# Kernel optimization log

Hardware: AMD Instinct MI355X
Metric: run time of the kernel (lower is better)

Reference implementation:

```python
import jax, jax.numpy as jnp
import numpy as np

B, CIN, COUT, T, K = 8, 64, 64, 16384, 127


def setup_inputs() -> dict:
    key = jax.random.key(0)
    kx, kw = jax.random.split(key)
    x = jax.random.normal(kx, (B, CIN, T), dtype=jnp.float32)
    sigma = np.sqrt(2.0 / (CIN * K + COUT)).astype(np.float32)
    W = jax.random.normal(kw, (COUT, CIN, K), dtype=jnp.float32) * sigma
    return {"x": x, "W": W}


def reference(x, W):
    # Full linear convolution via FFT (true convolution, matches
    # torchaudio.functional.fftconvolve), summed over in_channels,
    # then trimmed to mode='same' (output length == T, centered).
    T_ = x.shape[-1]
    K_ = W.shape[-1]
    n = T_ + K_ - 1  # linear-conv length, no circular wraparound
    Xf = jnp.fft.rfft(x, n=n)   # [B, Cin, nf] complex
    Wf = jnp.fft.rfft(W, n=n)   # [Cout, Cin, nf] complex
    # Batched complex multiply-accumulate over in_channels (single pass,
    # no per-output-channel redundant FFTs).
    Yf = jnp.einsum('bif,oif->bof', Xf, Wf)  # [B, Cout, nf]
    y_full = jnp.fft.irfft(Yf, n=n)          # [B, Cout, T+K-1]
    start = (K_ - 1) // 2                    # 'same': centered crop
    return y_full[..., start:start + T_]
```

## Files before the change

### kernel.cpp

```cpp
#include <hip/hip_runtime.h>

#define T_LEN 16384
#define CIN   64
#define COUT  64
#define KTAPS 127
#define TN    512
#define XROWS 640
#define WT_KS 4096

typedef __attribute__((ext_vector_type(8)))  __bf16 bf16x8;
typedef __attribute__((ext_vector_type(16))) float  f32x16;
typedef __attribute__((ext_vector_type(4)))  float  float4v;

__device__ inline unsigned short f2bf(float f) {
    unsigned u = __builtin_bit_cast(unsigned, f);
    u += 0x7fffu + ((u >> 16) & 1u);
    return (unsigned short)(u >> 16);
}

__global__ void wt_transform(const float* __restrict__ W,
                             unsigned short* __restrict__ Wt) {
    int tid = blockIdx.x * 256 + threadIdx.x;
    int o = tid >> 6, i = tid & 63;
    int cc = i >> 4, kg = (i >> 3) & 1, e = i & 7, m = o >> 5, l31 = o & 31;
    int hw = ((cc * 2 + m) * 64 + kg * 32 + l31) * 8 + e;
    const float* src = W + tid * KTAPS;
    unsigned short* dst = Wt + hw;
    for (int kp = 0; kp < KTAPS; ++kp)
        dst[kp * WT_KS] = f2bf(src[126 - kp]);
}

#define GLL16(g, l)                                                        \
    __builtin_amdgcn_global_load_lds(                                      \
        (const __attribute__((address_space(1))) void*)(g),                \
        (__attribute__((address_space(3))) void*)(l), 16, 0, 0)

__global__ __launch_bounds__(512, 2)
void conv_mfma(const float* __restrict__ x,
               const unsigned short* __restrict__ Wt,
               float* __restrict__ y) {
    __shared__ __align__(16) char pool[114688];
    unsigned short* xs = (unsigned short*)pool;
    char* asbase = pool + 81920;

    const int tid = threadIdx.x;
    const int bb  = blockIdx.x >> 5;
    const int tt  = blockIdx.x & 31;
    const int t0  = tt * TN;

    {
        const int cin = tid >> 3;
        const int s   = tid & 7;
        const float* xrow = x + (bb * CIN + cin) * T_LEN;
        const int p = cin >> 2, c3 = cin & 3;
        for (int j = 0; j < 20; ++j) {
            const int w = 32 * j + 4 * s;
            const int u = t0 - 64 + w;
            float4v v;
            if (u >= 0 && u + 4 <= T_LEN) {
                v = *(const float4v*)(xrow + u);
            } else {
                v.x = (u + 0 >= 0 && u + 0 < T_LEN) ? xrow[u + 0] : 0.f;
                v.y = (u + 1 >= 0 && u + 1 < T_LEN) ? xrow[u + 1] : 0.f;
                v.z = (u + 2 >= 0 && u + 2 < T_LEN) ? xrow[u + 2] : 0.f;
                v.w = (u + 3 >= 0 && u + 3 < T_LEN) ? xrow[u + 3] : 0.f;
            }
            #pragma unroll
            for (int e = 0; e < 4; ++e) {
                const int we = w + e;
                const float fv = (e == 0) ? v.x : (e == 1) ? v.y : (e == 2) ? v.z : v.w;
                xs[we * 64 + ((p ^ (we & 15)) << 2) + c3] = f2bf(fv);
            }
        }
    }

    auto stageA = [&](int k0, int k1, int buf) {
        #pragma unroll
        for (int h = 0; h < 2; ++h) {
            const int c   = tid + h * 512;
            const int q   = c >> 9;
            const int off = (c & 511) * 16;
            const char* g = (const char*)(Wt + (q ? k1 : k0) * WT_KS) + off;
            char* l = asbase + buf * 16384 + q * 8192 + off;
            GLL16(g, l);
        }
    };

    stageA(0, 64, 0);
    asm volatile("s_waitcnt vmcnt(0)" ::: "memory");
    __syncthreads();

    const int lane   = tid & 63;
    const int wv     = tid >> 6;
    const int quad   = wv >> 2;
    const int ww     = wv & 3;
    const int l31    = lane & 31;
    const int kg     = lane >> 5;
    const int twbase = ww * 128;
    const int brow0  = twbase + l31 + 1;

    f32x16 acc[2][4] = {};

    auto phase = [&](int p, int buf) {
        if (p + 1 < 64) {
            int k1 = 64 + p + 1; if (k1 > 126) k1 = 126;
            stageA(p + 1, k1, buf ^ 1);
        }
        const int kp = quad ? 64 + p : p;
        if (quad == 0 || p < 63) {
            const char* aslice = asbase + buf * 16384 + quad * 8192;
            const int rb   = brow0 + kp;
            const int rb15 = rb & 15;
            const char* xrowp = (const char*)xs + rb * 128;
            #pragma unroll
            for (int cc = 0; cc < 4; ++cc) {
                bf16x8 a0 = *(const bf16x8*)(aslice + ((cc * 2 + 0) * 64 + lane) * 16);
                bf16x8 a1 = *(const bf16x8*)(aslice + ((cc * 2 + 1) * 64 + lane) * 16);
                const int o0 = (((4 * cc + 2 * kg + 0) ^ rb15) << 3);
                const int o1 = (((4 * cc + 2 * kg + 1) ^ rb15) << 3);
                #pragma unroll
                for (int n = 0; n < 4; ++n) {
                    uint2 lo = *(const uint2*)(xrowp + n * 4096 + o0);
                    uint2 hi = *(const uint2*)(xrowp + n * 4096 + o1);
                    uint4 t4 = {lo.x, lo.y, hi.x, hi.y};
                    bf16x8 b = __builtin_bit_cast(bf16x8, t4);
                    acc[0][n] = __builtin_amdgcn_mfma_f32_32x32x16_bf16(a0, b, acc[0][n], 0, 0, 0);
                    acc[1][n] = __builtin_amdgcn_mfma_f32_32x32x16_bf16(a1, b, acc[1][n], 0, 0, 0);
                }
            }
        }
        asm volatile("s_waitcnt vmcnt(0)" ::: "memory");
        __builtin_amdgcn_s_barrier();
    };

    for (int p = 0; p < 64; p += 2) {
        phase(p + 0, 0);
        phase(p + 1, 1);
    }

    __syncthreads();
    float* msm = (float*)pool;
    #pragma unroll
    for (int m = 0; m < 2; ++m) {
        if (quad == 1) {
            #pragma unroll
            for (int n = 0; n < 4; ++n)
                #pragma unroll
                for (int r = 0; r < 16; ++r)
                    msm[(n * 16 + r) * 256 + ww * 64 + lane] = acc[m][n][r];
        }
        __syncthreads();
        if (quad == 0) {
            #pragma unroll
            for (int n = 0; n < 4; ++n)
                #pragma unroll
                for (int r = 0; r < 16; ++r)
                    acc[m][n][r] += msm[(n * 16 + r) * 256 + ww * 64 + lane];
        }
        __syncthreads();
    }

    if (quad == 0) {
        const int ybase = (bb * COUT) * T_LEN;
        #pragma unroll
        for (int m = 0; m < 2; ++m) {
            #pragma unroll
            for (int n = 0; n < 4; ++n) {
                const int t = t0 + twbase + n * 32 + l31;
                #pragma unroll
                for (int r = 0; r < 16; ++r) {
                    const int o = m * 32 + (r & 3) + 8 * (r >> 2) + 4 * kg;
                    y[ybase + o * T_LEN + t] = acc[m][n][r];
                }
            }
        }
    }
}

extern "C" void kernel_launch(void* const* d_in, const int* in_sizes, int n_in,
                              void* d_out, int out_size, void* d_ws, size_t ws_size,
                              hipStream_t stream) {
    const float* x = (const float*)d_in[0];
    const float* W = (const float*)d_in[1];
    float* yout = (float*)d_out;
    unsigned short* Wt = (unsigned short*)d_ws;

    wt_transform<<<16, 256, 0, stream>>>(W, Wt);

    const int grid = 8 * (T_LEN / TN);
    conv_mfma<<<grid, 512, 0, stream>>>(x, Wt, yout);
}
```

Before: 130.9 us.

## Load weight fragments directly to registers instead of staging through LDS

Replaces the LDS double-buffered weight staging (global_load_lds plus per-tap barriers) with direct global-to-register loads of the A fragments, double-buffered in registers across taps. This removes the per-tap workgroup barrier and the LDS A-buffer, shrinking shared memory. Each wave now issues its own global loads (duplicated across the four waves per quad), and more VGPRs are used, which may pressure occupancy under the 512x2 launch bound.

Result: faster. 125.9 us (-3.8%).

```diff
diff --git a/kernel.cpp b/kernel.cpp
--- a/kernel.cpp
+++ b/kernel.cpp
@@ -30,18 +30,12 @@
         dst[kp * WT_KS] = f2bf(src[126 - kp]);
 }
 
-#define GLL16(g, l)                                                        \
-    __builtin_amdgcn_global_load_lds(                                      \
-        (const __attribute__((address_space(1))) void*)(g),                \
-        (__attribute__((address_space(3))) void*)(l), 16, 0, 0)
-
 __global__ __launch_bounds__(512, 2)
 void conv_mfma(const float* __restrict__ x,
                const unsigned short* __restrict__ Wt,
                float* __restrict__ y) {
-    __shared__ __align__(16) char pool[114688];
+    __shared__ __align__(16) char pool[81920];
     unsigned short* xs = (unsigned short*)pool;
-    char* asbase = pool + 81920;
 
     const int tid = threadIdx.x;
     const int bb  = blockIdx.x >> 5;
@@ -74,22 +68,6 @@
         }
     }
 
-    auto stageA = [&](int k0, int k1, int buf) {
-        #pragma unroll
-        for (int h = 0; h < 2; ++h) {
-            const int c   = tid + h * 512;
-            const int q   = c >> 9;
-            const int off = (c & 511) * 16;
-            const char* g = (const char*)(Wt + (q ? k1 : k0) * WT_KS) + off;
-            char* l = asbase + buf * 16384 + q * 8192 + off;
-            GLL16(g, l);
-        }
-    };
-
-    stageA(0, 64, 0);
-    asm volatile("s_waitcnt vmcnt(0)" ::: "memory");
-    __syncthreads();
-
     const int lane   = tid & 63;
     const int wv     = tid >> 6;
     const int quad   = wv >> 2;
@@ -99,43 +77,48 @@
     const int twbase = ww * 128;
     const int brow0  = twbase + l31 + 1;
 
+    const int kp0  = quad ? 64 : 0;
+    const int ntap = quad ? 63 : 64;
+
+    const char* ab = (const char*)Wt + lane * 16;
+
     f32x16 acc[2][4] = {};
+    uint4 a0r[8], a1r[8];
 
-    auto phase = [&](int p, int buf) {
-        if (p + 1 < 64) {
-            int k1 = 64 + p + 1; if (k1 > 126) k1 = 126;
-            stageA(p + 1, k1, buf ^ 1);
-        }
-        const int kp = quad ? 64 + p : p;
-        if (quad == 0 || p < 63) {
-            const char* aslice = asbase + buf * 16384 + quad * 8192;
-            const int rb   = brow0 + kp;
-            const int rb15 = rb & 15;
-            const char* xrowp = (const char*)xs + rb * 128;
-            #pragma unroll
-            for (int cc = 0; cc < 4; ++cc) {
-                bf16x8 a0 = *(const bf16x8*)(aslice + ((cc * 2 + 0) * 64 + lane) * 16);
-                bf16x8 a1 = *(const bf16x8*)(aslice + ((cc * 2 + 1) * 64 + lane) * 16);
-                const int o0 = (((4 * cc + 2 * kg + 0) ^ rb15) << 3);
-                const int o1 = (((4 * cc + 2 * kg + 1) ^ rb15) << 3);
-                #pragma unroll
-                for (int n = 0; n < 4; ++n) {
-                    uint2 lo = *(const uint2*)(xrowp + n * 4096 + o0);
-                    uint2 hi = *(const uint2*)(xrowp + n * 4096 + o1);
-                    uint4 t4 = {lo.x, lo.y, hi.x, hi.y};
-                    bf16x8 b = __builtin_bit_cast(bf16x8, t4);
-                    acc[0][n] = __builtin_amdgcn_mfma_f32_32x32x16_bf16(a0, b, acc[0][n], 0, 0, 0);
-                    acc[1][n] = __builtin_amdgcn_mfma_f32_32x32x16_bf16(a1, b, acc[1][n], 0, 0, 0);
-                }
-            }
-        }
-        asm volatile("s_waitcnt vmcnt(0)" ::: "memory");
-        __builtin_amdgcn_s_barrier();
-    };
+    #define LOADA(dst, kp)                                                  \
+        {   const char* p_ = ab + (kp) * 8192;                              \
+            _Pragma("unroll")                                               \
+            for (int f = 0; f < 8; ++f)                                     \
+                dst[f] = *(const uint4*)(p_ + f * 1024); }
 
-    for (int p = 0; p < 64; p += 2) {
-        phase(p + 0, 0);
-        phase(p + 1, 1);
+    LOADA(a0r, kp0);
+    __syncthreads();
+
+    #define COMPUTE(ar, kp)                                                 \
+        {   const int rb_   = brow0 + (kp);                                 \
+            const int rb15_ = rb_ & 15;                                     \
+            const char* xrowp_ = (const char*)xs + rb_ * 128;               \
+            _Pragma("unroll")                                               \
+            for (int cc = 0; cc < 4; ++cc) {                                \
+                bf16x8 a0 = __builtin_bit_cast(bf16x8, ar[cc * 2 + 0]);     \
+                bf16x8 a1 = __builtin_bit_cast(bf16x8, ar[cc * 2 + 1]);     \
+                const int o0 = (((4 * cc + 2 * kg + 0) ^ rb15_) << 3);      \
+                const int o1 = (((4 * cc + 2 * kg + 1) ^ rb15_) << 3);      \
+                _Pragma("unroll")                                           \
+                for (int n = 0; n < 4; ++n) {                               \
+                    uint2 lo = *(const uint2*)(xrowp_ + n * 4096 + o0);     \
+                    uint2 hi = *(const uint2*)(xrowp_ + n * 4096 + o1);     \
+                    uint4 t4 = {lo.x, lo.y, hi.x, hi.y};                    \
+                    bf16x8 b = __builtin_bit_cast(bf16x8, t4);              \
+                    acc[0][n] = __builtin_amdgcn_mfma_f32_32x32x16_bf16(a0, b, acc[0][n], 0, 0, 0); \
+                    acc[1][n] = __builtin_amdgcn_mfma_f32_32x32x16_bf16(a1, b, acc[1][n], 0, 0, 0); \
+                } } }
+
+    for (int i = 0; i < ntap; i += 2) {
+        if (i + 1 < ntap) LOADA(a1r, kp0 + i + 1);
+        COMPUTE(a0r, kp0 + i);
+        if (i + 2 < ntap) LOADA(a0r, kp0 + i + 2);
+        if (i + 1 < ntap) COMPUTE(a1r, kp0 + i + 1);
     }
 
     __syncthreads();
```
